# Optimization experiments

Measured on AMD Instinct MI355X. Metric: run time of the kernel, lower is better.

## Reference

```python
import jax, jax.numpy as jnp
import numpy as np

INPUT_DIM = 16
HIDDEN = 64
N_RAW = INPUT_DIM - 3  # 13 raw features, last 3 are xyz coords


def setup_inputs() -> dict:
    key = jax.random.key(0)
    ks = jax.random.split(key, 16)
    B, N = 4, 512
    D = HIDDEN
    s = lambda fan_in: 1.0 / np.sqrt(fan_in)
    x = jax.random.normal(ks[0], (B, N, INPUT_DIM), dtype=jnp.float32)
    # feature projection [N_RAW -> D]
    Wf = jax.random.uniform(ks[1], (N_RAW, D), jnp.float32, -s(N_RAW), s(N_RAW))
    bf = jax.random.uniform(ks[2], (D,), jnp.float32, -s(N_RAW), s(N_RAW))
    # positional encoding MLP [3 -> D -> D]
    Wp1 = jax.random.uniform(ks[3], (3, D), jnp.float32, -s(3), s(3))
    bp1 = jax.random.uniform(ks[4], (D,), jnp.float32, -s(3), s(3))
    Wp2 = jax.random.uniform(ks[5], (D, D), jnp.float32, -s(D), s(D))
    bp2 = jax.random.uniform(ks[6], (D,), jnp.float32, -s(D), s(D))
    # node projection [D -> D]
    Wn = jax.random.uniform(ks[7], (D, D), jnp.float32, -s(D), s(D))
    bn = jax.random.uniform(ks[8], (D,), jnp.float32, -s(D), s(D))
    # edge MLP [2D -> D -> D//2 -> 1]
    W1 = jax.random.uniform(ks[9], (2 * D, D), jnp.float32, -s(2 * D), s(2 * D))
    b1 = jax.random.uniform(ks[10], (D,), jnp.float32, -s(2 * D), s(2 * D))
    W2 = jax.random.uniform(ks[11], (D, D // 2), jnp.float32, -s(D), s(D))
    b2 = jax.random.uniform(ks[12], (D // 2,), jnp.float32, -s(D), s(D))
    W3 = jax.random.uniform(ks[13], (D // 2, 1), jnp.float32, -s(D // 2), s(D // 2))
    b3 = jax.random.uniform(ks[14], (1,), jnp.float32, -s(D // 2), s(D // 2))
    return dict(x=x, Wf=Wf, bf=bf, Wp1=Wp1, bp1=bp1, Wp2=Wp2, bp2=bp2,
                Wn=Wn, bn=bn, W1=W1, b1=b1, W2=W2, b2=b2, W3=W3, b3=b3)


def reference(x, Wf, bf, Wp1, bp1, Wp2, bp2, Wn, bn, W1, b1, W2, b2, W3, b3):
    # split raw features / xyz coords
    feats = x[..., :N_RAW]           # [B,N,13]
    xyz = x[..., -3:]                # [B,N,3]
    pos = jax.nn.relu(xyz @ Wp1 + bp1) @ Wp2 + bp2
    proj = feats @ Wf + bf + pos     # [B,N,D]
    emb = proj @ Wn + bn             # [B,N,D] node embeddings
    # edge MLP layer1 on concat([u_i, u_j]): decompose W1 = [W1a; W1b].
    # cat([u_i,u_j]) @ W1 == u_i @ W1a + u_j @ W1b  (same math, no [B,N,N,2D])
    D = emb.shape[-1]
    a = emb @ W1[:D]                 # [B,N,D]
    b = emb @ W1[D:]                 # [B,N,D]
    h = jax.nn.relu(a[:, :, None, :] + b[:, None, :, :] + b1)  # [B,N,N,D]
    h = jax.nn.relu(h @ W2 + b2)     # [B,N,N,D//2]  (dropout = identity in eval)
    logits = (h @ W3 + b3)[..., 0]   # [B,N,N]
    return logits
```

## Files before the change

### kernel.cpp

```cpp
#include <hip/hip_runtime.h>
#include <stdint.h>

#define NPTS 512
#define NB 4
#define TJB 128
#define BST 72
#define SOST 40

typedef __attribute__((ext_vector_type(4))) float floatx4;
typedef __fp16 fp16x2 __attribute__((ext_vector_type(2)));
typedef _Float16 half2v __attribute__((ext_vector_type(2)));
typedef _Float16 half8v __attribute__((ext_vector_type(8)));

union H8 { fp16x2 p2[4]; half2v h2[4]; half8v h8; };

__global__ __launch_bounds__(256) void rows_kernel(
    const float* __restrict__ x,
    const float* __restrict__ Wf,  const float* __restrict__ bf,
    const float* __restrict__ Wp1, const float* __restrict__ bp1,
    const float* __restrict__ Wp2, const float* __restrict__ bp2,
    const float* __restrict__ Wn,  const float* __restrict__ bn,
    const float* __restrict__ W1,  const float* __restrict__ b1,
    _Float16* __restrict__ wsA, _Float16* __restrict__ wsB)
{
    __shared__ float posh[4][64];
    __shared__ float projS[4][64];
    __shared__ float embS[4][64];

    const int r   = threadIdx.x >> 6;
    const int t   = threadIdx.x & 63;
    const int row = blockIdx.x * 4 + r;
    const float* xr = x + row * 16;

    const float x13 = xr[13], x14 = xr[14], x15 = xr[15];
    float ph = x13 * Wp1[t] + x14 * Wp1[64 + t] + x15 * Wp1[128 + t] + bp1[t];
    posh[r][t] = fmaxf(ph, 0.f);
    __syncthreads();

    float s0 = 0.f, s1 = 0.f, s2 = 0.f, s3 = 0.f;
    #pragma unroll
    for (int k = 0; k < 64; k += 4) {
        s0 += posh[r][k    ] * Wp2[(k    ) * 64 + t];
        s1 += posh[r][k + 1] * Wp2[(k + 1) * 64 + t];
        s2 += posh[r][k + 2] * Wp2[(k + 2) * 64 + t];
        s3 += posh[r][k + 3] * Wp2[(k + 3) * 64 + t];
    }
    float acc = bp2[t] + ((s0 + s1) + (s2 + s3)) + bf[t];
    float f0 = 0.f, f1 = 0.f, f2 = 0.f, f3 = 0.f;
    #pragma unroll
    for (int k = 0; k < 12; k += 4) {
        f0 += xr[k    ] * Wf[(k    ) * 64 + t];
        f1 += xr[k + 1] * Wf[(k + 1) * 64 + t];
        f2 += xr[k + 2] * Wf[(k + 2) * 64 + t];
        f3 += xr[k + 3] * Wf[(k + 3) * 64 + t];
    }
    acc += ((f0 + f1) + (f2 + f3)) + xr[12] * Wf[12 * 64 + t];
    projS[r][t] = acc;
    __syncthreads();

    float e0 = 0.f, e1 = 0.f, e2 = 0.f, e3 = 0.f;
    #pragma unroll
    for (int k = 0; k < 64; k += 4) {
        e0 += projS[r][k    ] * Wn[(k    ) * 64 + t];
        e1 += projS[r][k + 1] * Wn[(k + 1) * 64 + t];
        e2 += projS[r][k + 2] * Wn[(k + 2) * 64 + t];
        e3 += projS[r][k + 3] * Wn[(k + 3) * 64 + t];
    }
    embS[r][t] = bn[t] + ((e0 + e1) + (e2 + e3));
    __syncthreads();

    float a0 = 0.f, a1 = 0.f, a2 = 0.f, a3 = 0.f;
    float v0 = 0.f, v1 = 0.f, v2 = 0.f, v3 = 0.f;
    #pragma unroll
    for (int k = 0; k < 64; k += 4) {
        const float g0 = embS[r][k], g1 = embS[r][k + 1], g2 = embS[r][k + 2], g3 = embS[r][k + 3];
        a0 += g0 * W1[(k    ) * 64 + t];
        a1 += g1 * W1[(k + 1) * 64 + t];
        a2 += g2 * W1[(k + 2) * 64 + t];
        a3 += g3 * W1[(k + 3) * 64 + t];
        v0 += g0 * W1[(64 + k    ) * 64 + t];
        v1 += g1 * W1[(64 + k + 1) * 64 + t];
        v2 += g2 * W1[(64 + k + 2) * 64 + t];
        v3 += g3 * W1[(64 + k + 3) * 64 + t];
    }
    wsA[row * 64 + t] = (_Float16)(b1[t] + ((a0 + a1) + (a2 + a3)));
    wsB[row * 64 + t] = (_Float16)((v0 + v1) + (v2 + v3));
}

__global__ __launch_bounds__(256) void pairs_kernel(
    const _Float16* __restrict__ wsA, const _Float16* __restrict__ wsB,
    const float* __restrict__ W2,  const float* __restrict__ b2,
    const float* __restrict__ W3,  const float* __restrict__ b3,
    float* __restrict__ out)
{
    __shared__ _Float16 bS[TJB][BST];
    __shared__ _Float16 sO[4][2][16][SOST];

    const int tid = threadIdx.x;
    const int w   = tid >> 6;
    const int l   = tid & 63;
    const int q   = l >> 4;
    const int c   = l & 15;
    const int q8  = q * 8;

    const int bidx = blockIdx.x;
    const int jt = bidx & 3;
    const int ig = (bidx >> 2) & 63;
    const int bb = bidx >> 8;
    const int j0 = jt * TJB;
    const int i0 = ig * 8 + w * 2;

    const _Float16* bG = wsB + (bb * NPTS + j0) * 64;
    #pragma unroll
    for (int p = 0; p < 4; ++p) {
        const int flat = p * 256 + tid;
        const int rr = flat >> 3, ch = (flat & 7) * 8;
        *(half8v*)&bS[rr][ch] = *(const half8v*)(bG + rr * 64 + ch);
    }

    half8v Wf16[2][2];
    #pragma unroll
    for (int kt = 0; kt < 2; ++kt)
        #pragma unroll
        for (int nt = 0; nt < 2; ++nt) {
            H8 u;
            #pragma unroll
            for (int e = 0; e < 8; ++e)
                u.h8[e] = (_Float16)W2[(kt * 32 + q8 + e) * 32 + nt * 16 + c];
            Wf16[kt][nt] = u.h8;
        }

    half8v w3f;
    #pragma unroll
    for (int e = 0; e < 8; ++e) {
        const int p = q8 + e;
        w3f[e] = (_Float16)W3[(p >> 1) + ((p & 1) << 4)];
    }

    const float b2c = b2[c], b2c16 = b2[c + 16];
    const float b3v = b3[0];

    const _Float16* aG0 = wsA + (bb * NPTS + i0) * 64;
    const _Float16* aG1 = aG0 + 64;
    const half8v aA0 = *(const half8v*)(aG0 + q8);
    const half8v aA1 = *(const half8v*)(aG0 + 32 + q8);
    const half8v aB0 = *(const half8v*)(aG1 + q8);
    const half8v aB1 = *(const half8v*)(aG1 + 32 + q8);
    const half8v zero8 = (half8v)(_Float16)0.0f;

    __syncthreads();

    float* orow0 = out + ((size_t)(bb * NPTS + i0)) * NPTS + j0;
    float* orow1 = orow0 + NPTS;

    #pragma unroll 2
    for (int mt = 0; mt < 8; ++mt) {
        const int m = mt * 16 + c;
        const half8v b0v = *(const half8v*)&bS[m][q8];
        const half8v b1v = *(const half8v*)&bS[m][32 + q8];

        const half8v hA0 = __builtin_elementwise_max(aA0 + b0v, zero8);
        const half8v hA1 = __builtin_elementwise_max(aA1 + b1v, zero8);
        const half8v hB0 = __builtin_elementwise_max(aB0 + b0v, zero8);
        const half8v hB1 = __builtin_elementwise_max(aB1 + b1v, zero8);

        floatx4 aA0c = {b2c, b2c, b2c, b2c};
        floatx4 aA1c = {b2c16, b2c16, b2c16, b2c16};
        floatx4 aB0c = aA0c, aB1c = aA1c;
        aA0c = __builtin_amdgcn_mfma_f32_16x16x32_f16(hA0, Wf16[0][0], aA0c, 0, 0, 0);
        aA0c = __builtin_amdgcn_mfma_f32_16x16x32_f16(hA1, Wf16[1][0], aA0c, 0, 0, 0);
        aA1c = __builtin_amdgcn_mfma_f32_16x16x32_f16(hA0, Wf16[0][1], aA1c, 0, 0, 0);
        aA1c = __builtin_amdgcn_mfma_f32_16x16x32_f16(hA1, Wf16[1][1], aA1c, 0, 0, 0);
        aB0c = __builtin_amdgcn_mfma_f32_16x16x32_f16(hB0, Wf16[0][0], aB0c, 0, 0, 0);
        aB0c = __builtin_amdgcn_mfma_f32_16x16x32_f16(hB1, Wf16[1][0], aB0c, 0, 0, 0);
        aB1c = __builtin_amdgcn_mfma_f32_16x16x32_f16(hB0, Wf16[0][1], aB1c, 0, 0, 0);
        aB1c = __builtin_amdgcn_mfma_f32_16x16x32_f16(hB1, Wf16[1][1], aB1c, 0, 0, 0);

        #pragma unroll
        for (int r = 0; r < 4; ++r) {
            H8 pkA, pkB;
            pkA.p2[0] = __builtin_amdgcn_cvt_pkrtz(aA0c[r], aA1c[r]);
            pkA.h2[0] = __builtin_elementwise_max(pkA.h2[0], (half2v)(_Float16)0.0f);
            *(half2v*)&sO[w][0][q * 4 + r][2 * c] = pkA.h2[0];
            pkB.p2[0] = __builtin_amdgcn_cvt_pkrtz(aB0c[r], aB1c[r]);
            pkB.h2[0] = __builtin_elementwise_max(pkB.h2[0], (half2v)(_Float16)0.0f);
            *(half2v*)&sO[w][1][q * 4 + r][2 * c] = pkB.h2[0];
        }
        const half8v arA = *(const half8v*)&sO[w][0][c][q8];
        const half8v arB = *(const half8v*)&sO[w][1][c][q8];

        floatx4 dlA = {b3v, b3v, b3v, b3v};
        floatx4 dlB = {b3v, b3v, b3v, b3v};
        dlA = __builtin_amdgcn_mfma_f32_16x16x32_f16(arA, w3f, dlA, 0, 0, 0);
        dlB = __builtin_amdgcn_mfma_f32_16x16x32_f16(arB, w3f, dlB, 0, 0, 0);

        const float lgA = (c == 0) ? dlA[0] : ((c == 1) ? dlA[1] : ((c == 2) ? dlA[2] : dlA[3]));
        const float lgB = (c == 0) ? dlB[0] : ((c == 1) ? dlB[1] : ((c == 2) ? dlB[2] : dlB[3]));
        if (c < 4) {
            orow0[mt * 16 + q * 4 + c] = lgA;
            orow1[mt * 16 + q * 4 + c] = lgB;
        }
    }
}

extern "C" void kernel_launch(void* const* d_in, const int* in_sizes, int n_in,
                              void* d_out, int out_size, void* d_ws, size_t ws_size,
                              hipStream_t stream) {
    const float* x   = (const float*)d_in[0];
    const float* Wf  = (const float*)d_in[1];
    const float* bf  = (const float*)d_in[2];
    const float* Wp1 = (const float*)d_in[3];
    const float* bp1 = (const float*)d_in[4];
    const float* Wp2 = (const float*)d_in[5];
    const float* bp2 = (const float*)d_in[6];
    const float* Wn  = (const float*)d_in[7];
    const float* bn  = (const float*)d_in[8];
    const float* W1  = (const float*)d_in[9];
    const float* b1  = (const float*)d_in[10];
    const float* W2  = (const float*)d_in[11];
    const float* b2  = (const float*)d_in[12];
    const float* W3  = (const float*)d_in[13];
    const float* b3  = (const float*)d_in[14];

    _Float16* wsA = (_Float16*)d_ws;
    _Float16* wsB = wsA + NB * NPTS * 64;

    rows_kernel<<<NB * NPTS / 4, 256, 0, stream>>>(
        x, Wf, bf, Wp1, bp1, Wp2, bp2, Wn, bn, W1, b1, wsA, wsB);

    pairs_kernel<<<NB * 64 * 4, 256, 0, stream>>>(
        wsA, wsB, W2, b2, W3, b3, (float*)d_out);
}
```

Before: 97.34 us.

## Fuse row and pair kernels into one cooperative kernel with grid sync

Merges the per-row embedding kernel and the pairwise edge-MLP kernel into a single cooperative launch. Each block computes two rows of wsA/wsB (splitting the K reduction across half-blocks), then all blocks meet at a grid-wide barrier before running the MFMA pair stage. The goal is to remove the second kernel launch and the gap between kernels, at the cost of a grid sync, a union-shared-memory layout and a requirement that all 1024 blocks be co-resident. If the cooperative launch fails, it falls back to the original two kernels.

```diff
diff --git a/kernel.cpp b/kernel.cpp
--- a/kernel.cpp
+++ b/kernel.cpp
@@ -1,5 +1,8 @@
 #include <hip/hip_runtime.h>
+#include <hip/hip_cooperative_groups.h>
 #include <stdint.h>
+
+namespace cg = cooperative_groups;
 
 #define NPTS 512
 #define NB 4
@@ -13,6 +16,206 @@
 typedef _Float16 half8v __attribute__((ext_vector_type(8)));
 
 union H8 { fp16x2 p2[4]; half2v h2[4]; half8v h8; };
+
+union SMem {
+    struct { _Float16 bS[TJB][BST]; _Float16 sO[4][2][16][SOST]; } p;
+    struct { float posh[2][64]; float red[2][2][64];
+             float projS[2][64]; float embS[2][64]; } r;
+};
+
+__global__ __launch_bounds__(256, 4) void fused_kernel(
+    const float* __restrict__ x,
+    const float* __restrict__ Wf,  const float* __restrict__ bf,
+    const float* __restrict__ Wp1, const float* __restrict__ bp1,
+    const float* __restrict__ Wp2, const float* __restrict__ bp2,
+    const float* __restrict__ Wn,  const float* __restrict__ bn,
+    const float* __restrict__ W1,  const float* __restrict__ b1,
+    const float* __restrict__ W2,  const float* __restrict__ b2,
+    const float* __restrict__ W3,  const float* __restrict__ b3,
+    float* __restrict__ out,
+    _Float16* __restrict__ wsA, _Float16* __restrict__ wsB)
+{
+    __shared__ SMem sm;
+    const int tid = threadIdx.x;
+
+    {
+        const int r2  = tid >> 7;
+        const int kh  = (tid >> 6) & 1;
+        const int t   = tid & 63;
+        const int row = blockIdx.x * 2 + r2;
+        const float* xr = x + row * 16;
+        const int k0 = kh << 5;
+
+        {
+            const float x13 = xr[13], x14 = xr[14], x15 = xr[15];
+            float ph = x13 * Wp1[t] + x14 * Wp1[64 + t] + x15 * Wp1[128 + t] + bp1[t];
+            if (kh == 0) sm.r.posh[r2][t] = fmaxf(ph, 0.f);
+        }
+        __syncthreads();
+
+        {
+            float s0 = 0.f, s1 = 0.f, s2 = 0.f, s3 = 0.f;
+            #pragma unroll
+            for (int k = 0; k < 32; k += 4) {
+                s0 += sm.r.posh[r2][k0 + k    ] * Wp2[(k0 + k    ) * 64 + t];
+                s1 += sm.r.posh[r2][k0 + k + 1] * Wp2[(k0 + k + 1) * 64 + t];
+                s2 += sm.r.posh[r2][k0 + k + 2] * Wp2[(k0 + k + 2) * 64 + t];
+                s3 += sm.r.posh[r2][k0 + k + 3] * Wp2[(k0 + k + 3) * 64 + t];
+            }
+            float part = (s0 + s1) + (s2 + s3);
+            if (kh == 0) {
+                #pragma unroll
+                for (int k = 0; k < 6; ++k) part += xr[k] * Wf[k * 64 + t];
+            } else {
+                #pragma unroll
+                for (int k = 6; k < 13; ++k) part += xr[k] * Wf[k * 64 + t];
+            }
+            sm.r.red[r2][kh][t] = part;
+        }
+        __syncthreads();
+        if (kh == 0)
+            sm.r.projS[r2][t] = sm.r.red[r2][0][t] + sm.r.red[r2][1][t] + bp2[t] + bf[t];
+        __syncthreads();
+
+        {
+            float e0 = 0.f, e1 = 0.f, e2 = 0.f, e3 = 0.f;
+            #pragma unroll
+            for (int k = 0; k < 32; k += 4) {
+                e0 += sm.r.projS[r2][k0 + k    ] * Wn[(k0 + k    ) * 64 + t];
+                e1 += sm.r.projS[r2][k0 + k + 1] * Wn[(k0 + k + 1) * 64 + t];
+                e2 += sm.r.projS[r2][k0 + k + 2] * Wn[(k0 + k + 2) * 64 + t];
+                e3 += sm.r.projS[r2][k0 + k + 3] * Wn[(k0 + k + 3) * 64 + t];
+            }
+            sm.r.red[r2][kh][t] = (e0 + e1) + (e2 + e3);
+        }
+        __syncthreads();
+        if (kh == 0)
+            sm.r.embS[r2][t] = sm.r.red[r2][0][t] + sm.r.red[r2][1][t] + bn[t];
+        __syncthreads();
+
+        {
+            const float* Wbase = W1 + (kh ? 64 * 64 : 0);
+            float a0 = 0.f, a1 = 0.f, a2 = 0.f, a3 = 0.f;
+            #pragma unroll
+            for (int k = 0; k < 64; k += 4) {
+                a0 += sm.r.embS[r2][k    ] * Wbase[(k    ) * 64 + t];
+                a1 += sm.r.embS[r2][k + 1] * Wbase[(k + 1) * 64 + t];
+                a2 += sm.r.embS[r2][k + 2] * Wbase[(k + 2) * 64 + t];
+                a3 += sm.r.embS[r2][k + 3] * Wbase[(k + 3) * 64 + t];
+            }
+            const float resv = (a0 + a1) + (a2 + a3);
+            if (kh == 0) wsA[row * 64 + t] = (_Float16)(resv + b1[t]);
+            else         wsB[row * 64 + t] = (_Float16)resv;
+        }
+    }
+
+    const int w   = tid >> 6;
+    const int l   = tid & 63;
+    const int q   = l >> 4;
+    const int c   = l & 15;
+    const int q8  = q * 8;
+
+    const int bidx = blockIdx.x;
+    const int jt = bidx & 3;
+    const int ig = (bidx >> 2) & 63;
+    const int bb = bidx >> 8;
+    const int j0 = jt * TJB;
+    const int i0 = ig * 8 + w * 2;
+
+    half8v Wf16[2][2];
+    #pragma unroll
+    for (int kt = 0; kt < 2; ++kt)
+        #pragma unroll
+        for (int nt = 0; nt < 2; ++nt) {
+            H8 u;
+            #pragma unroll
+            for (int e = 0; e < 8; ++e)
+                u.h8[e] = (_Float16)W2[(kt * 32 + q8 + e) * 32 + nt * 16 + c];
+            Wf16[kt][nt] = u.h8;
+        }
+
+    half8v w3f;
+    #pragma unroll
+    for (int e = 0; e < 8; ++e) {
+        const int p = q8 + e;
+        w3f[e] = (_Float16)W3[(p >> 1) + ((p & 1) << 4)];
+    }
+
+    const float b2c = b2[c], b2c16 = b2[c + 16];
+    const float b3v = b3[0];
+    const half8v zero8 = (half8v)(_Float16)0.0f;
+
+    cg::this_grid().sync();
+
+    const _Float16* bG = wsB + (bb * NPTS + j0) * 64;
+    #pragma unroll
+    for (int pgi = 0; pgi < 4; ++pgi) {
+        const int flat = pgi * 256 + tid;
+        const int rr = flat >> 3, ch = (flat & 7) * 8;
+        *(half8v*)&sm.p.bS[rr][ch] = *(const half8v*)(bG + rr * 64 + ch);
+    }
+
+    const _Float16* aG0 = wsA + (bb * NPTS + i0) * 64;
+    const _Float16* aG1 = aG0 + 64;
+    const half8v aA0 = *(const half8v*)(aG0 + q8);
+    const half8v aA1 = *(const half8v*)(aG0 + 32 + q8);
+    const half8v aB0 = *(const half8v*)(aG1 + q8);
+    const half8v aB1 = *(const half8v*)(aG1 + 32 + q8);
+
+    __syncthreads();
+
+    float* orow0 = out + ((size_t)(bb * NPTS + i0)) * NPTS + j0;
+    float* orow1 = orow0 + NPTS;
+
+    #pragma unroll 2
+    for (int mt = 0; mt < 8; ++mt) {
+        const int m = mt * 16 + c;
+        const half8v b0v = *(const half8v*)&sm.p.bS[m][q8];
+        const half8v b1v = *(const half8v*)&sm.p.bS[m][32 + q8];
+
+        const half8v hA0 = __builtin_elementwise_max(aA0 + b0v, zero8);
+        const half8v hA1 = __builtin_elementwise_max(aA1 + b1v, zero8);
+        const half8v hB0 = __builtin_elementwise_max(aB0 + b0v, zero8);
+        const half8v hB1 = __builtin_elementwise_max(aB1 + b1v, zero8);
+
+        floatx4 aA0c = {b2c, b2c, b2c, b2c};
+        floatx4 aA1c = {b2c16, b2c16, b2c16, b2c16};
+        floatx4 aB0c = aA0c, aB1c = aA1c;
+        aA0c = __builtin_amdgcn_mfma_f32_16x16x32_f16(hA0, Wf16[0][0], aA0c, 0, 0, 0);
+        aA0c = __builtin_amdgcn_mfma_f32_16x16x32_f16(hA1, Wf16[1][0], aA0c, 0, 0, 0);
+        aA1c = __builtin_amdgcn_mfma_f32_16x16x32_f16(hA0, Wf16[0][1], aA1c, 0, 0, 0);
+        aA1c = __builtin_amdgcn_mfma_f32_16x16x32_f16(hA1, Wf16[1][1], aA1c, 0, 0, 0);
+        aB0c = __builtin_amdgcn_mfma_f32_16x16x32_f16(hB0, Wf16[0][0], aB0c, 0, 0, 0);
+        aB0c = __builtin_amdgcn_mfma_f32_16x16x32_f16(hB1, Wf16[1][0], aB0c, 0, 0, 0);
+        aB1c = __builtin_amdgcn_mfma_f32_16x16x32_f16(hB0, Wf16[0][1], aB1c, 0, 0, 0);
+        aB1c = __builtin_amdgcn_mfma_f32_16x16x32_f16(hB1, Wf16[1][1], aB1c, 0, 0, 0);
+
+        #pragma unroll
+        for (int r = 0; r < 4; ++r) {
+            H8 pkA, pkB;
+            pkA.p2[0] = __builtin_amdgcn_cvt_pkrtz(aA0c[r], aA1c[r]);
+            pkA.h2[0] = __builtin_elementwise_max(pkA.h2[0], (half2v)(_Float16)0.0f);
+            *(half2v*)&sm.p.sO[w][0][q * 4 + r][2 * c] = pkA.h2[0];
+            pkB.p2[0] = __builtin_amdgcn_cvt_pkrtz(aB0c[r], aB1c[r]);
+            pkB.h2[0] = __builtin_elementwise_max(pkB.h2[0], (half2v)(_Float16)0.0f);
+            *(half2v*)&sm.p.sO[w][1][q * 4 + r][2 * c] = pkB.h2[0];
+        }
+        const half8v arA = *(const half8v*)&sm.p.sO[w][0][c][q8];
+        const half8v arB = *(const half8v*)&sm.p.sO[w][1][c][q8];
+
+        floatx4 dlA = {b3v, b3v, b3v, b3v};
+        floatx4 dlB = {b3v, b3v, b3v, b3v};
+        dlA = __builtin_amdgcn_mfma_f32_16x16x32_f16(arA, w3f, dlA, 0, 0, 0);
+        dlB = __builtin_amdgcn_mfma_f32_16x16x32_f16(arB, w3f, dlB, 0, 0, 0);
+
+        const float lgA = (c == 0) ? dlA[0] : ((c == 1) ? dlA[1] : ((c == 2) ? dlA[2] : dlA[3]));
+        const float lgB = (c == 0) ? dlB[0] : ((c == 1) ? dlB[1] : ((c == 2) ? dlB[2] : dlB[3]));
+        if (c < 4) {
+            orow0[mt * 16 + q * 4 + c] = lgA;
+            orow1[mt * 16 + q * 4 + c] = lgB;
+        }
+    }
+}
 
 __global__ __launch_bounds__(256) void rows_kernel(
     const float* __restrict__ x,
@@ -224,10 +427,19 @@
 
     _Float16* wsA = (_Float16*)d_ws;
     _Float16* wsB = wsA + NB * NPTS * 64;
-
-    rows_kernel<<<NB * NPTS / 4, 256, 0, stream>>>(
-        x, Wf, bf, Wp1, bp1, Wp2, bp2, Wn, bn, W1, b1, wsA, wsB);
-
-    pairs_kernel<<<NB * 64 * 4, 256, 0, stream>>>(
-        wsA, wsB, W2, b2, W3, b3, (float*)d_out);
+    float* outp   = (float*)d_out;
+
+    void* args[] = { (void*)&x, (void*)&Wf, (void*)&bf, (void*)&Wp1, (void*)&bp1,
+                     (void*)&Wp2, (void*)&bp2, (void*)&Wn, (void*)&bn,
+                     (void*)&W1, (void*)&b1, (void*)&W2, (void*)&b2,
+                     (void*)&W3, (void*)&b3, (void*)&outp, (void*)&wsA, (void*)&wsB };
+    hipError_t err = hipLaunchCooperativeKernel((void*)fused_kernel,
+                                                dim3(NB * 64 * 4), dim3(256),
+                                                args, 0, stream);
+    if (err != hipSuccess) {
+        rows_kernel<<<NB * NPTS / 4, 256, 0, stream>>>(
+            x, Wf, bf, Wp1, bp1, Wp2, bp2, Wn, bn, W1, b1, wsA, wsB);
+        pairs_kernel<<<NB * 64 * 4, 256, 0, stream>>>(
+            wsA, wsB, W2, b2, W3, b3, (float*)d_out);
+    }
 }
```

Result: slower. 214.2 us (+120.1%).
